# Kernel optimization log

Measured on AMD Instinct MI355X. Metric: run time of the kernel, lower is better.

The kernel has to match this reference:

```python
import jax, jax.numpy as jnp
import numpy as np


def setup_inputs() -> dict:
    key = jax.random.key(0)
    k1, k2, k3 = jax.random.split(key, 3)
    B, S, H, Dk = 4, 1024, 16, 4
    E = H * Dk
    return {
        "x": jax.random.normal(k1, (B, S, E), dtype=jnp.float32),
        "theta": jax.random.normal(k2, (Dk,), dtype=jnp.float32),  # heads[0] RY params, shared by all heads (bug in source reproduced)
        "W": jax.random.normal(k3, (E, E), dtype=jnp.float32) / np.sqrt(E),
        "b": jnp.zeros((E,), dtype=jnp.float32),
    }


def reference(x, theta, W, b):
    # x: [B, S, E], E = H * 4
    B, S, E = x.shape
    Dk = 4
    H = E // Dk
    inv_sqrt_dk = 1.0 / np.float32(np.sqrt(Dk))

    # 4-qubit circuit per token/head, no entangling gates -> each wire independent:
    #   |0> --RX(x_i)--RY(theta_i)--  <PauliZ> = cos(theta_i) * cos(x_i)
    # (exact closed form of the torchquantum statevector simulation)
    # chunk along embed dim == reshape [B, S, H, Dk]
    proj = jnp.cos(x.reshape(B, S, H, Dk)) * jnp.cos(theta)  # theta broadcasts over wires
    proj = proj.transpose(0, 2, 1, 3)  # [B, H, S, Dk]

    scores = jnp.einsum('bhsd,bhtd->bhst', proj, proj) * inv_sqrt_dk  # [B, H, S, S]
    attn = jax.nn.softmax(scores, axis=-1)  # dropout = identity in eval mode
    out = jnp.einsum('bhst,bhtd->bhsd', attn, proj)  # [B, H, S, Dk]

    out = out.transpose(0, 2, 1, 3).reshape(B, S, E)  # [B, S, E]
    return out @ W.T + b
```

## Files before the change

kernel.cpp:

```cpp
#include <hip/hip_runtime.h>
#include <hip/hip_bf16.h>

#define SQ 1024
#define HH 16
#define DK 4
#define EE 64

using short8 = __attribute__((ext_vector_type(8))) short;
using f32x4  = __attribute__((ext_vector_type(4))) float;
using us4    = __attribute__((ext_vector_type(4))) unsigned short;
using us8    = __attribute__((ext_vector_type(8))) unsigned short;

static __device__ inline unsigned short f2bf(float f) {
  return __builtin_bit_cast(unsigned short, __float2bfloat16(f));
}

__global__ __launch_bounds__(1024) void qattn_mfma(
    const float* __restrict__ x, const float* __restrict__ theta,
    float* __restrict__ y) {
  const int tid = threadIdx.x;
  const int quarter = blockIdx.x & 3;
  const int bh = blockIdx.x >> 2;
  const int hd = bh & (HH - 1);
  const int b = bh >> 4;

  __shared__ __align__(16) unsigned short afrag[32][16][8];
  __shared__ __align__(16) unsigned short vfrag[32][4][5][8];
  __shared__ __align__(16) unsigned short qfrag[256][4];
  __shared__ __align__(16) unsigned short zslot[8];

  const float4 th = *reinterpret_cast<const float4*>(theta);
  const float ct[4] = {__cosf(th.x), __cosf(th.y), __cosf(th.z), __cosf(th.w)};
  const float sc = 0.5f * 1.4426950408889634f;
  const int q_lo = quarter * 256;

  if (tid < 8) zslot[tid] = 0;
  vfrag[tid >> 5][(tid >> 3) & 3][4][tid & 7] = 0x3F80;

  const float* xb = x + ((size_t)b * SQ) * EE + hd * DK;
  {
    const int t = tid;
    const float4 v = *reinterpret_cast<const float4*>(xb + (size_t)t * EE);
    const float p[4] = {__cosf(v.x) * ct[0], __cosf(v.y) * ct[1],
                        __cosf(v.z) * ct[2], __cosf(v.w) * ct[3]};
    unsigned short pb[4], qb[4];
#pragma unroll
    for (int d = 0; d < 4; ++d) {
      pb[d] = f2bf(p[d]);
      qb[d] = f2bf(p[d] * sc);
    }
    const int c = t >> 5, tl = t & 31, hq = tl >> 3, j = tl & 7;
    *reinterpret_cast<us4*>(&afrag[c][4 * hq + (j & 3)][(j >= 4) ? 4 : 0]) =
        (us4){pb[0], pb[1], pb[2], pb[3]};
#pragma unroll
    for (int nn = 0; nn < 4; ++nn) vfrag[c][hq][nn][j] = pb[nn];
    const int ql = t - q_lo;
    if ((unsigned)ql < 256u)
      *reinterpret_cast<us4*>(&qfrag[ql][0]) = (us4){qb[0], qb[1], qb[2], qb[3]};
  }
  __syncthreads();

  const int lane = tid & 63;
  const int wid = tid >> 6;
  const int n = lane & 15, hg = lane >> 4;

  short8 qf = {0, 0, 0, 0, 0, 0, 0, 0};
  {
    const unsigned short* qa =
        (lane < 16) ? &qfrag[wid * 16 + n][0] : &zslot[0];
    const us4 ta = *reinterpret_cast<const us4*>(qa);
#pragma unroll
    for (int i = 0; i < 4; ++i) qf[i] = (short)ta[i];
  }

  const unsigned short* aptr = (lane < 16) ? &afrag[0][n][0] : &zslot[0];
  const int astep = (lane < 16) ? 128 : 0;
  const unsigned short* vptr = (n <= 4) ? &vfrag[0][hg][n][0] : &zslot[0];
  const int vstep = (n <= 4) ? 160 : 0;

  f32x4 acc = {0.f, 0.f, 0.f, 0.f};
  const f32x4 zero = {0.f, 0.f, 0.f, 0.f};

#pragma unroll 4
  for (int c = 0; c < 32; ++c) {
    const us8 av = *reinterpret_cast<const us8*>(aptr + c * astep);
    const short8 A1 = {(short)av[0], (short)av[1], (short)av[2], (short)av[3],
                       0, 0, 0, 0};
    const short8 A2 = {(short)av[4], (short)av[5], (short)av[6], (short)av[7],
                       0, 0, 0, 0};
    const f32x4 s1 = __builtin_amdgcn_mfma_f32_16x16x32_bf16(A1, qf, zero, 0, 0, 0);
    const f32x4 s2 = __builtin_amdgcn_mfma_f32_16x16x32_bf16(A2, qf, zero, 0, 0, 0);

    short8 PA;
#pragma unroll
    for (int r = 0; r < 4; ++r) {
      PA[r]     = (short)f2bf(__builtin_amdgcn_exp2f(s1[r]));
      PA[r + 4] = (short)f2bf(__builtin_amdgcn_exp2f(s2[r]));
    }

    const us8 vv = *reinterpret_cast<const us8*>(vptr + c * vstep);
    const short8 VB = __builtin_bit_cast(short8, vv);
    acc = __builtin_amdgcn_mfma_f32_16x16x32_bf16(PA, VB, acc, 0, 0, 0);
  }

  const int qbase = q_lo + wid * 16;
#pragma unroll
  for (int r = 0; r < 4; ++r) {
    const float den = __shfl(acc[r], (lane & 48) | 4, 64);
    const float val = acc[r] * (1.0f / den);
    if (n < 4) {
      y[((size_t)(b * SQ + qbase + 4 * hg + r)) * EE + hd * DK + n] = val;
    }
  }
}

__global__ __launch_bounds__(256) void proj_kernel(
    const float* __restrict__ y, const float* __restrict__ W,
    const float* __restrict__ bias, float* __restrict__ out) {
  const int tid = threadIdx.x;
  __shared__ float Wt[EE][68];
  __shared__ float yt[16][68];

  const float4* W4 = reinterpret_cast<const float4*>(W);
#pragma unroll
  for (int k = 0; k < 4; ++k) {
    const int i4 = tid + k * 256;
    const float4 w = W4[i4];
    const int e = i4 >> 4;
    const int j0 = (i4 & 15) * 4;
    Wt[j0 + 0][e] = w.x; Wt[j0 + 1][e] = w.y;
    Wt[j0 + 2][e] = w.z; Wt[j0 + 3][e] = w.w;
  }
  const size_t tok0 = (size_t)blockIdx.x * 16;
  {
    const float4 v = reinterpret_cast<const float4*>(y + tok0 * EE)[tid];
    *reinterpret_cast<float4*>(&yt[tid >> 4][(tid & 15) * 4]) = v;
  }
  __syncthreads();

  const int t = tid >> 4;
  const int eg = tid & 15;
  const int e0 = eg * 4;
  f32x4 acc = *reinterpret_cast<const f32x4*>(bias + e0);
#pragma unroll
  for (int jq = 0; jq < 16; ++jq) {
    const f32x4 yv = *reinterpret_cast<const f32x4*>(&yt[t][jq * 4]);
    const f32x4 w0 = *reinterpret_cast<const f32x4*>(&Wt[jq * 4 + 0][e0]);
    const f32x4 w1 = *reinterpret_cast<const f32x4*>(&Wt[jq * 4 + 1][e0]);
    const f32x4 w2 = *reinterpret_cast<const f32x4*>(&Wt[jq * 4 + 2][e0]);
    const f32x4 w3 = *reinterpret_cast<const f32x4*>(&Wt[jq * 4 + 3][e0]);
    acc += yv[0] * w0 + yv[1] * w1 + yv[2] * w2 + yv[3] * w3;
  }
  *reinterpret_cast<f32x4*>(&out[((size_t)tok0 + t) * EE + e0]) = acc;
}

extern "C" void kernel_launch(void* const* d_in, const int* in_sizes, int n_in,
                              void* d_out, int out_size, void* d_ws, size_t ws_size,
                              hipStream_t stream) {
  const float* x     = (const float*)d_in[0];
  const float* theta = (const float*)d_in[1];
  const float* W     = (const float*)d_in[2];
  const float* bias  = (const float*)d_in[3];
  float* out = (float*)d_out;
  float* y   = (float*)d_ws;

  qattn_mfma<<<256, 1024, 0, stream>>>(x, theta, y);
  proj_kernel<<<256, 256, 0, stream>>>(y, W, bias, out);
}
```

Before: 19.66 us.

## Process two query tiles per wave with half the threads and truncating bf16 pack

Halves the attention block to 512 threads, with each wave now handling 32 queries using two Q fragments. The key fragment and V loads are shared across both tiles, and the staging loop runs twice per thread. It also swaps round-to-nearest bf16 conversion for a single perm-based truncating pack. It adds a constant shift to the score accumulator init, which acts as a softmax offset that cancels on normalisation. The aim is less LDS traffic and conversion overhead per MFMA, at the cost of lower occupancy and reduced bf16 rounding accuracy.

Measured after the change: 20.23 us. +2.9%, slower.

```diff
diff --git a/kernel.cpp b/kernel.cpp
--- a/kernel.cpp
+++ b/kernel.cpp
@@ -10,12 +10,19 @@
 using f32x4  = __attribute__((ext_vector_type(4))) float;
 using us4    = __attribute__((ext_vector_type(4))) unsigned short;
 using us8    = __attribute__((ext_vector_type(8))) unsigned short;
+using u32x4  = __attribute__((ext_vector_type(4))) unsigned;
 
 static __device__ inline unsigned short f2bf(float f) {
   return __builtin_bit_cast(unsigned short, __float2bfloat16(f));
 }
 
-__global__ __launch_bounds__(1024) void qattn_mfma(
+static __device__ inline unsigned trunc_pk_bf16(float lo, float hi) {
+  return __builtin_amdgcn_perm(__builtin_bit_cast(unsigned, hi),
+                               __builtin_bit_cast(unsigned, lo),
+                               0x07060302u);
+}
+
+__global__ __launch_bounds__(512) void qattn_mfma(
     const float* __restrict__ x, const float* __restrict__ theta,
     float* __restrict__ y) {
   const int tid = threadIdx.x;
@@ -35,11 +42,16 @@
   const int q_lo = quarter * 256;
 
   if (tid < 8) zslot[tid] = 0;
-  vfrag[tid >> 5][(tid >> 3) & 3][4][tid & 7] = 0x3F80;
+#pragma unroll
+  for (int k = 0; k < 2; ++k) {
+    const int e = tid + k * 512;
+    vfrag[e >> 5][(e >> 3) & 3][4][e & 7] = 0x3F80;
+  }
 
   const float* xb = x + ((size_t)b * SQ) * EE + hd * DK;
-  {
-    const int t = tid;
+#pragma unroll
+  for (int k = 0; k < 2; ++k) {
+    const int t = tid + k * 512;
     const float4 v = *reinterpret_cast<const float4*>(xb + (size_t)t * EE);
     const float p[4] = {__cosf(v.x) * ct[0], __cosf(v.y) * ct[1],
                         __cosf(v.z) * ct[2], __cosf(v.w) * ct[3]};
@@ -64,13 +76,16 @@
   const int wid = tid >> 6;
   const int n = lane & 15, hg = lane >> 4;
 
-  short8 qf = {0, 0, 0, 0, 0, 0, 0, 0};
+  short8 qf0 = {0, 0, 0, 0, 0, 0, 0, 0}, qf1 = qf0;
   {
     const unsigned short* qa =
-        (lane < 16) ? &qfrag[wid * 16 + n][0] : &zslot[0];
+        (lane < 16) ? &qfrag[wid * 32 + n][0] : &zslot[0];
+    const unsigned short* qb2 =
+        (lane < 16) ? &qfrag[wid * 32 + 16 + n][0] : &zslot[0];
     const us4 ta = *reinterpret_cast<const us4*>(qa);
-#pragma unroll
-    for (int i = 0; i < 4; ++i) qf[i] = (short)ta[i];
+    const us4 tb = *reinterpret_cast<const us4*>(qb2);
+#pragma unroll
+    for (int i = 0; i < 4; ++i) { qf0[i] = (short)ta[i]; qf1[i] = (short)tb[i]; }
   }
 
   const unsigned short* aptr = (lane < 16) ? &afrag[0][n][0] : &zslot[0];
@@ -78,38 +93,59 @@
   const unsigned short* vptr = (n <= 4) ? &vfrag[0][hg][n][0] : &zslot[0];
   const int vstep = (n <= 4) ? 160 : 0;
 
-  f32x4 acc = {0.f, 0.f, 0.f, 0.f};
-  const f32x4 zero = {0.f, 0.f, 0.f, 0.f};
-
-#pragma unroll 4
+  f32x4 acc0 = {0.f, 0.f, 0.f, 0.f}, acc1 = acc0;
+  const float csh = 0.0056245491938781f;
+  const f32x4 cc = {csh, csh, csh, csh};
+
+#pragma unroll 2
   for (int c = 0; c < 32; ++c) {
     const us8 av = *reinterpret_cast<const us8*>(aptr + c * astep);
     const short8 A1 = {(short)av[0], (short)av[1], (short)av[2], (short)av[3],
                        0, 0, 0, 0};
     const short8 A2 = {(short)av[4], (short)av[5], (short)av[6], (short)av[7],
                        0, 0, 0, 0};
-    const f32x4 s1 = __builtin_amdgcn_mfma_f32_16x16x32_bf16(A1, qf, zero, 0, 0, 0);
-    const f32x4 s2 = __builtin_amdgcn_mfma_f32_16x16x32_bf16(A2, qf, zero, 0, 0, 0);
-
-    short8 PA;
-#pragma unroll
-    for (int r = 0; r < 4; ++r) {
-      PA[r]     = (short)f2bf(__builtin_amdgcn_exp2f(s1[r]));
-      PA[r + 4] = (short)f2bf(__builtin_amdgcn_exp2f(s2[r]));
-    }
+    const f32x4 s1a = __builtin_amdgcn_mfma_f32_16x16x32_bf16(A1, qf0, cc, 0, 0, 0);
+    const f32x4 s2a = __builtin_amdgcn_mfma_f32_16x16x32_bf16(A2, qf0, cc, 0, 0, 0);
+    const f32x4 s1b = __builtin_amdgcn_mfma_f32_16x16x32_bf16(A1, qf1, cc, 0, 0, 0);
+    const f32x4 s2b = __builtin_amdgcn_mfma_f32_16x16x32_bf16(A2, qf1, cc, 0, 0, 0);
+
+    u32x4 p0, p1;
+    p0[0] = trunc_pk_bf16(__builtin_amdgcn_exp2f(s1a[0]),
+                          __builtin_amdgcn_exp2f(s1a[1]));
+    p0[1] = trunc_pk_bf16(__builtin_amdgcn_exp2f(s1a[2]),
+                          __builtin_amdgcn_exp2f(s1a[3]));
+    p0[2] = trunc_pk_bf16(__builtin_amdgcn_exp2f(s2a[0]),
+                          __builtin_amdgcn_exp2f(s2a[1]));
+    p0[3] = trunc_pk_bf16(__builtin_amdgcn_exp2f(s2a[2]),
+                          __builtin_amdgcn_exp2f(s2a[3]));
+    p1[0] = trunc_pk_bf16(__builtin_amdgcn_exp2f(s1b[0]),
+                          __builtin_amdgcn_exp2f(s1b[1]));
+    p1[1] = trunc_pk_bf16(__builtin_amdgcn_exp2f(s1b[2]),
+                          __builtin_amdgcn_exp2f(s1b[3]));
+    p1[2] = trunc_pk_bf16(__builtin_amdgcn_exp2f(s2b[0]),
+                          __builtin_amdgcn_exp2f(s2b[1]));
+    p1[3] = trunc_pk_bf16(__builtin_amdgcn_exp2f(s2b[2]),
+                          __builtin_amdgcn_exp2f(s2b[3]));
+    const short8 PA0 = __builtin_bit_cast(short8, p0);
+    const short8 PA1 = __builtin_bit_cast(short8, p1);
 
     const us8 vv = *reinterpret_cast<const us8*>(vptr + c * vstep);
     const short8 VB = __builtin_bit_cast(short8, vv);
-    acc = __builtin_amdgcn_mfma_f32_16x16x32_bf16(PA, VB, acc, 0, 0, 0);
-  }
-
-  const int qbase = q_lo + wid * 16;
-#pragma unroll
-  for (int r = 0; r < 4; ++r) {
-    const float den = __shfl(acc[r], (lane & 48) | 4, 64);
-    const float val = acc[r] * (1.0f / den);
-    if (n < 4) {
-      y[((size_t)(b * SQ + qbase + 4 * hg + r)) * EE + hd * DK + n] = val;
+    acc0 = __builtin_amdgcn_mfma_f32_16x16x32_bf16(PA0, VB, acc0, 0, 0, 0);
+    acc1 = __builtin_amdgcn_mfma_f32_16x16x32_bf16(PA1, VB, acc1, 0, 0, 0);
+  }
+
+#pragma unroll
+  for (int half = 0; half < 2; ++half) {
+    const f32x4 acc = half ? acc1 : acc0;
+    const int qbase = q_lo + wid * 32 + half * 16;
+#pragma unroll
+    for (int r = 0; r < 4; ++r) {
+      const float den = __shfl(acc[r], (lane & 48) | 4, 64);
+      const float val = acc[r] * (1.0f / den);
+      if (n < 4) {
+        y[((size_t)(b * SQ + qbase + 4 * hg + r)) * EE + hd * DK + n] = val;
+      }
     }
   }
 }
@@ -164,6 +200,6 @@
   float* out = (float*)d_out;
   float* y   = (float*)d_ws;
 
-  qattn_mfma<<<256, 1024, 0, stream>>>(x, theta, y);
+  qattn_mfma<<<256, 512, 0, stream>>>(x, theta, y);
   proj_kernel<<<256, 256, 0, stream>>>(y, W, bias, out);
 }
```
